# Performance work log

Measured on AMD Instinct MI355X. Metric: run time of the kernel, lower is better.

The kernel has to match this reference:

```python
import jax, jax.numpy as jnp
import numpy as np

H = 64          # heightmap size (sqrt of in_channels=4096)
FEATS = [8, 16, 32, 64]
NEG_SLOPE = 0.01
EPS = 1e-12


def setup_inputs() -> dict:
    key = jax.random.key(0)
    ks = jax.random.split(key, 32)
    inp = {"x": jax.random.normal(ks[0], (16384, H * H), dtype=jnp.float32)}
    in_feat = H
    ki = 1
    for li, out_feat in enumerate(FEATS):
        bound = np.sqrt(6.0 / (in_feat + out_feat))  # xavier_uniform
        inp[f"w{li}"] = jax.random.uniform(ks[ki], (out_feat, in_feat), minval=-bound, maxval=bound, dtype=jnp.float32); ki += 1
        inp[f"b{li}"] = jnp.zeros((out_feat,), dtype=jnp.float32)
        inp[f"s{li}"] = jnp.ones((1,), dtype=jnp.float32)  # sigma parameter
        in_feat = out_feat
    compress_in = H * FEATS[-1]
    inp["wm0"] = jax.random.normal(ks[ki], (80, compress_in), dtype=jnp.float32) * 0.02; ki += 1
    inp["bm0"] = jnp.zeros((80,), dtype=jnp.float32)
    inp["wm1"] = jax.random.normal(ks[ki], (60, 80), dtype=jnp.float32) * 0.02; ki += 1
    inp["bm1"] = jnp.zeros((60,), dtype=jnp.float32)
    return inp


def _gauss_layer(x, dist_sq, sigma, w, b):
    # x: [B, H, Cin] ; dist_sq: [H, H] ; w: [Cout, Cin]
    xp = jnp.einsum('bhc,oc->bho', x, w) + b
    k = jnp.exp(-dist_sq / (2.0 * sigma[0] ** 2))                 # [H, H]
    k = k / jnp.maximum(jnp.sum(k, axis=-1, keepdims=True), EPS)  # L1 normalize
    out = jnp.einsum('ij,bjc->bic', k, xp)
    return jax.nn.leaky_relu(out, NEG_SLOPE)


def reference(x, w0, b0, s0, w1, b1, s1, w2, b2, s2, w3, b3, s3, wm0, bm0, wm1, bm1):
    B = x.shape[0]
    h = x.reshape(B, H, H)
    idx = jnp.arange(H, dtype=x.dtype)
    dist_sq = (idx[:, None] - idx[None, :]) ** 2  # coords are 1-D row indices
    for sigma, w, b in ((s0, w0, b0), (s1, w1, b1), (s2, w2, b2), (s3, w3, b3)):
        h = _gauss_layer(h, dist_sq, sigma, w, b)
    h = h.reshape(B, -1)                              # [B, H*64]
    h = jax.nn.leaky_relu(h @ wm0.T + bm0, NEG_SLOPE)
    h = jax.nn.leaky_relu(h @ wm1.T + bm1, NEG_SLOPE)
    return h
```

## Files before the change

kernel.cpp:

```cpp
#include <hip/hip_runtime.h>


typedef _Float16 f16x8 __attribute__((ext_vector_type(8)));
typedef _Float16 f16x4 __attribute__((ext_vector_type(4)));
typedef float    f32x4 __attribute__((ext_vector_type(4)));

#define KT_OFF    327680
#define W0P_OFF   344064
#define W1P_OFF   345088
#define W2P_OFF   345600
#define W3P_OFF   346624

__global__ void prep_all(const float* __restrict__ s0, const float* __restrict__ s1,
                         const float* __restrict__ s2, const float* __restrict__ s3,
                         const float* __restrict__ w0, const float* __restrict__ w1,
                         const float* __restrict__ w2, const float* __restrict__ w3,
                         const float* __restrict__ wm0, _Float16* __restrict__ base) {
  int bid = blockIdx.x, tid = threadIdx.x;
  if (bid < 1280) {
    int idx = bid * 256 + tid;
    int kc = idx / 2560, rem = idx % 2560;
    int n = rem >> 5, o = rem & 31;
    base[idx] = (_Float16)wm0[n * 4096 + kc * 32 + o];
  } else if (bid == 1280) {
    int li = tid >> 6, i = tid & 63;
    float sg = (li == 0) ? s0[0] : (li == 1) ? s1[0] : (li == 2) ? s2[0] : s3[0];
    float denom = 2.0f * sg * sg;
    float sum = 0.0f;
    for (int j = 0; j < 64; ++j) {
      float d = (float)(i - j);
      sum += expf(-(d * d) / denom);
    }
    float inv = 1.0f / fmaxf(sum, 1e-12f);
    for (int j = 0; j < 64; ++j) {
      float d = (float)(i - j);
      base[KT_OFF + (li * 64 + i) * 64 + j] = (_Float16)(expf(-(d * d) / denom) * inv);
    }
  } else {
    for (int r = tid; r < 4608; r += 256) {
      float v;
      if (r < 1024)      { int o = r >> 6, c = r & 63;             v = (o < 8)  ? w0[o * 64 + c] : 0.0f; }
      else if (r < 1536) { int q = r - 1024; int o = q >> 5, c = q & 31; v = (c < 8)  ? w1[o * 8 + c]  : 0.0f; }
      else if (r < 2560) { int q = r - 1536; int o = q >> 5, c = q & 31; v = (c < 16) ? w2[o * 16 + c] : 0.0f; }
      else               { int q = r - 2560; int o = q >> 5, c = q & 31; v = w3[o * 32 + c]; }
      base[W0P_OFF + r] = (_Float16)v;
    }
  }
}

__device__ __forceinline__ float leaky(float v) { return v > 0.0f ? v : 0.01f * v; }

__device__ __forceinline__ int swz(int sx, int row, int c) {
  return row * 64 + ((((c >> 3) ^ (row & 7) ^ sx) & 7) << 3) + (c & 7);
}

template<int NT, int KC, int KPAD>
__device__ __forceinline__ void stage_a(_Float16* __restrict__ P, int sx,
                                        const _Float16* __restrict__ wp, const float* bv,
                                        int lo, int hi) {
  f16x8 a[4][KC];
#pragma unroll
  for (int mt = 0; mt < 4; ++mt)
#pragma unroll
    for (int kc = 0; kc < KC; ++kc)
      a[mt][kc] = *(const f16x8*)(P + swz(sx, mt * 16 + lo, kc * 32 + hi * 8));
  f16x8 wf[NT][KC];
#pragma unroll
  for (int nt = 0; nt < NT; ++nt)
#pragma unroll
    for (int kc = 0; kc < KC; ++kc)
      wf[nt][kc] = *(const f16x8*)(wp + (nt * 16 + lo) * KPAD + kc * 32 + hi * 8);
#pragma unroll
  for (int mt = 0; mt < 4; ++mt)
#pragma unroll
    for (int nt = 0; nt < NT; ++nt) {
      f32x4 acc = {0.0f, 0.0f, 0.0f, 0.0f};
#pragma unroll
      for (int kc = 0; kc < KC; ++kc)
        acc = __builtin_amdgcn_mfma_f32_16x16x32_f16(a[mt][kc], wf[nt][kc], acc, 0, 0, 0);
      f16x4 hv;
#pragma unroll
      for (int r = 0; r < 4; ++r) hv[r] = (_Float16)(acc[r] + bv[nt]);
      *(f16x4*)(P + swz(sx, nt * 16 + lo, mt * 16 + hi * 4)) = hv;
    }
}

template<int MT>
__device__ __forceinline__ void stage_b(_Float16* __restrict__ P, int sx,
                                        const _Float16* __restrict__ kmat, int lo, int hi) {
  f16x8 ax[MT][2];
#pragma unroll
  for (int ot = 0; ot < MT; ++ot)
#pragma unroll
    for (int kc = 0; kc < 2; ++kc)
      ax[ot][kc] = *(const f16x8*)(P + swz(sx, ot * 16 + lo, kc * 32 + hi * 8));
  f16x8 kb[4][2];
#pragma unroll
  for (int nt = 0; nt < 4; ++nt)
#pragma unroll
    for (int kc = 0; kc < 2; ++kc)
      kb[nt][kc] = *(const f16x8*)(kmat + (nt * 16 + lo) * 64 + kc * 32 + hi * 8);
#pragma unroll
  for (int ot = 0; ot < MT; ++ot)
#pragma unroll
    for (int nt = 0; nt < 4; ++nt) {
      f32x4 acc = {0.0f, 0.0f, 0.0f, 0.0f};
#pragma unroll
      for (int kc = 0; kc < 2; ++kc)
        acc = __builtin_amdgcn_mfma_f32_16x16x32_f16(ax[ot][kc], kb[nt][kc], acc, 0, 0, 0);
      f16x4 hv;
#pragma unroll
      for (int r = 0; r < 4; ++r) hv[r] = (_Float16)leaky(acc[r]);
      *(f16x4*)(P + swz(sx, nt * 16 + lo, ot * 16 + hi * 4)) = hv;
    }
}

__global__ __launch_bounds__(512, 4)
void fused(const float* __restrict__ x,
           const float* __restrict__ bb0, const float* __restrict__ bb1,
           const float* __restrict__ bb2, const float* __restrict__ bb3,
           const _Float16* __restrict__ wsh,
           const float* __restrict__ bm0, const float* __restrict__ wm1,
           const float* __restrict__ bm1, float* __restrict__ out, int B) {
  __shared__ _Float16 lds[8][4096];
  const int tid = threadIdx.x;
  const int wv = tid >> 6, lane = tid & 63;
  const int lo = lane & 15, hi = lane >> 4;
  const int smp0 = blockIdx.x * 8;
  int smp = smp0 + wv;
  if (smp >= B) smp = B - 1;
  _Float16* P = lds[wv];
  const int sx = wv;

  float bv0 = (lo < 8) ? bb0[lo] : 0.0f;
  float bv1 = bb1[lo];
  float bv2[2] = {bb2[lo], bb2[16 + lo]};
  float bv3[4] = {bb3[lo], bb3[16 + lo], bb3[32 + lo], bb3[48 + lo]};

  const float4* xv = (const float4*)(x + (size_t)smp * 4096);
#pragma unroll
  for (int t = 0; t < 16; ++t) {
    float4 v = xv[t * 64 + lane];
    f16x4 hv;
    hv[0] = (_Float16)v.x; hv[1] = (_Float16)v.y; hv[2] = (_Float16)v.z; hv[3] = (_Float16)v.w;
    *(f16x4*)(P + swz(sx, t * 4 + hi, lo * 4)) = hv;
  }

  const _Float16* kt = wsh + KT_OFF;
  stage_a<1, 2, 64>(P, sx, wsh + W0P_OFF, &bv0, lo, hi);
  stage_b<1>(P, sx, kt + 0 * 4096, lo, hi);
  stage_a<1, 1, 32>(P, sx, wsh + W1P_OFF, &bv1, lo, hi);
  stage_b<1>(P, sx, kt + 1 * 4096, lo, hi);
  stage_a<2, 1, 32>(P, sx, wsh + W2P_OFF, bv2, lo, hi);
  stage_b<2>(P, sx, kt + 2 * 4096, lo, hi);
  stage_a<4, 1, 32>(P, sx, wsh + W3P_OFF, bv3, lo, hi);
  stage_b<4>(P, sx, kt + 3 * 4096, lo, hi);

  __syncthreads();

  f32x4 acc[5];
#pragma unroll
  for (int nt = 0; nt < 5; ++nt) { f32x4 z = {0.0f, 0.0f, 0.0f, 0.0f}; acc[nt] = z; }

  const _Float16* ap = &lds[lo & 7][0];
#pragma unroll 2
  for (int it = 0; it < 16; ++it) {
    int kc = wv * 16 + it;
    int row = kc >> 1, cc = (kc & 1) * 32 + hi * 8;
    f16x8 a = *(const f16x8*)(ap + swz(lo & 7, row, cc));
    const _Float16* bp = wsh + (size_t)kc * 2560 + lo * 32 + hi * 8;
#pragma unroll
    for (int nt = 0; nt < 5; ++nt) {
      f16x8 b = *(const f16x8*)(bp + nt * 512);
      acc[nt] = __builtin_amdgcn_mfma_f32_16x16x32_f16(a, b, acc[nt], 0, 0, 0);
    }
  }
  __syncthreads();

  float* scr = (float*)&lds[0][0];
  if (hi < 2) {
#pragma unroll
    for (int nt = 0; nt < 5; ++nt)
#pragma unroll
      for (int r = 0; r < 4; ++r)
        scr[wv * 640 + (hi * 4 + r) * 80 + nt * 16 + lo] = acc[nt][r];
  }
  __syncthreads();

  float* h1 = scr + 5120;
  for (int e = tid; e < 640; e += 512) {
    int m = e / 80, n = e - m * 80;
    float v = bm0[n];
#pragma unroll
    for (int w = 0; w < 8; ++w) v += scr[w * 640 + e];
    h1[e] = leaky(v);
  }
  __syncthreads();

  if (tid < 480) {
    int m = tid / 60, n = tid - m * 60;
    float v = bm1[n];
    const float4* hr = (const float4*)(h1 + m * 80);
    const float4* wr = (const float4*)(wm1 + n * 80);
#pragma unroll
    for (int k2 = 0; k2 < 20; ++k2) {
      float4 hv = hr[k2], wv4 = wr[k2];
      v += hv.x * wv4.x + hv.y * wv4.y + hv.z * wv4.z + hv.w * wv4.w;
    }
    int s = smp0 + m;
    if (s < B) out[(size_t)s * 60 + n] = leaky(v);
  }
}

extern "C" void kernel_launch(void* const* d_in, const int* in_sizes, int n_in,
                              void* d_out, int out_size, void* d_ws, size_t ws_size,
                              hipStream_t stream) {
  const float* x   = (const float*)d_in[0];
  const float* w0  = (const float*)d_in[1];
  const float* b0  = (const float*)d_in[2];
  const float* s0  = (const float*)d_in[3];
  const float* w1  = (const float*)d_in[4];
  const float* b1  = (const float*)d_in[5];
  const float* s1  = (const float*)d_in[6];
  const float* w2  = (const float*)d_in[7];
  const float* b2  = (const float*)d_in[8];
  const float* s2  = (const float*)d_in[9];
  const float* w3  = (const float*)d_in[10];
  const float* b3  = (const float*)d_in[11];
  const float* s3  = (const float*)d_in[12];
  const float* wm0 = (const float*)d_in[13];
  const float* bm0 = (const float*)d_in[14];
  const float* wm1 = (const float*)d_in[15];
  const float* bm1 = (const float*)d_in[16];
  float* out = (float*)d_out;
  _Float16* wsh = (_Float16*)d_ws;

  int B = in_sizes[0] / 4096;

  prep_all<<<1282, 256, 0, stream>>>(s0, s1, s2, s3, w0, w1, w2, w3, wm0, wsh);
  fused<<<(B + 7) / 8, 512, 0, stream>>>(x, b0, b1, b2, b3, wsh, bm0, wm1, bm1, out, B);
}
```

Baseline: 189.0 us.

## Split each sample's Gauss-layer chain across two waves with block barriers

Blocks grow to 1024 threads so two wavefronts share each sample. Each wave does half the x load, half the output tiles of every projection and smoothing stage, and half the compress-GEMM k-chunks. Block-wide barriers around every stage keep the shared LDS buffer consistent. The aim is more parallelism per sample and shorter per-wave register and latency chains, at the cost of many extra __syncthreads per block and reduced blocks per CU.

```diff
diff --git a/kernel.cpp b/kernel.cpp
--- a/kernel.cpp
+++ b/kernel.cpp
@@ -55,67 +55,71 @@
 }
 
 template<int NT, int KC, int KPAD>
-__device__ __forceinline__ void stage_a(_Float16* __restrict__ P, int sx,
-                                        const _Float16* __restrict__ wp, const float* bv,
-                                        int lo, int hi) {
-  f16x8 a[4][KC];
-#pragma unroll
-  for (int mt = 0; mt < 4; ++mt)
+__device__ __forceinline__ void stage_a2(_Float16* __restrict__ P, int sx, int half,
+                                         const _Float16* __restrict__ wp, const float* bv,
+                                         int lo, int hi) {
+  f16x8 a[2][KC];
+#pragma unroll
+  for (int m = 0; m < 2; ++m)
 #pragma unroll
     for (int kc = 0; kc < KC; ++kc)
-      a[mt][kc] = *(const f16x8*)(P + swz(sx, mt * 16 + lo, kc * 32 + hi * 8));
+      a[m][kc] = *(const f16x8*)(P + swz(sx, (half * 2 + m) * 16 + lo, kc * 32 + hi * 8));
   f16x8 wf[NT][KC];
 #pragma unroll
   for (int nt = 0; nt < NT; ++nt)
 #pragma unroll
     for (int kc = 0; kc < KC; ++kc)
       wf[nt][kc] = *(const f16x8*)(wp + (nt * 16 + lo) * KPAD + kc * 32 + hi * 8);
-#pragma unroll
-  for (int mt = 0; mt < 4; ++mt)
+  __syncthreads();
+#pragma unroll
+  for (int m = 0; m < 2; ++m)
 #pragma unroll
     for (int nt = 0; nt < NT; ++nt) {
       f32x4 acc = {0.0f, 0.0f, 0.0f, 0.0f};
 #pragma unroll
       for (int kc = 0; kc < KC; ++kc)
-        acc = __builtin_amdgcn_mfma_f32_16x16x32_f16(a[mt][kc], wf[nt][kc], acc, 0, 0, 0);
+        acc = __builtin_amdgcn_mfma_f32_16x16x32_f16(a[m][kc], wf[nt][kc], acc, 0, 0, 0);
       f16x4 hv;
 #pragma unroll
       for (int r = 0; r < 4; ++r) hv[r] = (_Float16)(acc[r] + bv[nt]);
-      *(f16x4*)(P + swz(sx, nt * 16 + lo, mt * 16 + hi * 4)) = hv;
-    }
+      *(f16x4*)(P + swz(sx, nt * 16 + lo, (half * 2 + m) * 16 + hi * 4)) = hv;
+    }
+  __syncthreads();
 }
 
 template<int MT>
-__device__ __forceinline__ void stage_b(_Float16* __restrict__ P, int sx,
-                                        const _Float16* __restrict__ kmat, int lo, int hi) {
+__device__ __forceinline__ void stage_b2(_Float16* __restrict__ P, int sx, int half,
+                                         const _Float16* __restrict__ kmat, int lo, int hi) {
   f16x8 ax[MT][2];
 #pragma unroll
   for (int ot = 0; ot < MT; ++ot)
 #pragma unroll
     for (int kc = 0; kc < 2; ++kc)
       ax[ot][kc] = *(const f16x8*)(P + swz(sx, ot * 16 + lo, kc * 32 + hi * 8));
-  f16x8 kb[4][2];
-#pragma unroll
-  for (int nt = 0; nt < 4; ++nt)
+  f16x8 kb[2][2];
+#pragma unroll
+  for (int n = 0; n < 2; ++n)
 #pragma unroll
     for (int kc = 0; kc < 2; ++kc)
-      kb[nt][kc] = *(const f16x8*)(kmat + (nt * 16 + lo) * 64 + kc * 32 + hi * 8);
+      kb[n][kc] = *(const f16x8*)(kmat + ((half * 2 + n) * 16 + lo) * 64 + kc * 32 + hi * 8);
+  __syncthreads();
 #pragma unroll
   for (int ot = 0; ot < MT; ++ot)
 #pragma unroll
-    for (int nt = 0; nt < 4; ++nt) {
+    for (int n = 0; n < 2; ++n) {
       f32x4 acc = {0.0f, 0.0f, 0.0f, 0.0f};
 #pragma unroll
       for (int kc = 0; kc < 2; ++kc)
-        acc = __builtin_amdgcn_mfma_f32_16x16x32_f16(ax[ot][kc], kb[nt][kc], acc, 0, 0, 0);
+        acc = __builtin_amdgcn_mfma_f32_16x16x32_f16(ax[ot][kc], kb[n][kc], acc, 0, 0, 0);
       f16x4 hv;
 #pragma unroll
       for (int r = 0; r < 4; ++r) hv[r] = (_Float16)leaky(acc[r]);
-      *(f16x4*)(P + swz(sx, nt * 16 + lo, ot * 16 + hi * 4)) = hv;
-    }
-}
-
-__global__ __launch_bounds__(512, 4)
+      *(f16x4*)(P + swz(sx, (half * 2 + n) * 16 + lo, ot * 16 + hi * 4)) = hv;
+    }
+  __syncthreads();
+}
+
+__global__ __launch_bounds__(1024, 6)
 void fused(const float* __restrict__ x,
            const float* __restrict__ bb0, const float* __restrict__ bb1,
            const float* __restrict__ bb2, const float* __restrict__ bb3,
@@ -126,11 +130,12 @@
   const int tid = threadIdx.x;
   const int wv = tid >> 6, lane = tid & 63;
   const int lo = lane & 15, hi = lane >> 4;
+  const int sample = wv >> 1, half = wv & 1;
   const int smp0 = blockIdx.x * 8;
-  int smp = smp0 + wv;
+  int smp = smp0 + sample;
   if (smp >= B) smp = B - 1;
-  _Float16* P = lds[wv];
-  const int sx = wv;
+  _Float16* P = lds[sample];
+  const int sx = sample;
 
   float bv0 = (lo < 8) ? bb0[lo] : 0.0f;
   float bv1 = bb1[lo];
@@ -139,24 +144,24 @@
 
   const float4* xv = (const float4*)(x + (size_t)smp * 4096);
 #pragma unroll
-  for (int t = 0; t < 16; ++t) {
+  for (int tt = 0; tt < 8; ++tt) {
+    int t = half * 8 + tt;
     float4 v = xv[t * 64 + lane];
     f16x4 hv;
     hv[0] = (_Float16)v.x; hv[1] = (_Float16)v.y; hv[2] = (_Float16)v.z; hv[3] = (_Float16)v.w;
     *(f16x4*)(P + swz(sx, t * 4 + hi, lo * 4)) = hv;
   }
+  __syncthreads();
 
   const _Float16* kt = wsh + KT_OFF;
-  stage_a<1, 2, 64>(P, sx, wsh + W0P_OFF, &bv0, lo, hi);
-  stage_b<1>(P, sx, kt + 0 * 4096, lo, hi);
-  stage_a<1, 1, 32>(P, sx, wsh + W1P_OFF, &bv1, lo, hi);
-  stage_b<1>(P, sx, kt + 1 * 4096, lo, hi);
-  stage_a<2, 1, 32>(P, sx, wsh + W2P_OFF, bv2, lo, hi);
-  stage_b<2>(P, sx, kt + 2 * 4096, lo, hi);
-  stage_a<4, 1, 32>(P, sx, wsh + W3P_OFF, bv3, lo, hi);
-  stage_b<4>(P, sx, kt + 3 * 4096, lo, hi);
-
-  __syncthreads();
+  stage_a2<1, 2, 64>(P, sx, half, wsh + W0P_OFF, &bv0, lo, hi);
+  stage_b2<1>(P, sx, half, kt + 0 * 4096, lo, hi);
+  stage_a2<1, 1, 32>(P, sx, half, wsh + W1P_OFF, &bv1, lo, hi);
+  stage_b2<1>(P, sx, half, kt + 1 * 4096, lo, hi);
+  stage_a2<2, 1, 32>(P, sx, half, wsh + W2P_OFF, bv2, lo, hi);
+  stage_b2<2>(P, sx, half, kt + 2 * 4096, lo, hi);
+  stage_a2<4, 1, 32>(P, sx, half, wsh + W3P_OFF, bv3, lo, hi);
+  stage_b2<4>(P, sx, half, kt + 3 * 4096, lo, hi);
 
   f32x4 acc[5];
 #pragma unroll
@@ -164,8 +169,8 @@
 
   const _Float16* ap = &lds[lo & 7][0];
 #pragma unroll 2
-  for (int it = 0; it < 16; ++it) {
-    int kc = wv * 16 + it;
+  for (int it = 0; it < 8; ++it) {
+    int kc = wv * 8 + it;
     int row = kc >> 1, cc = (kc & 1) * 32 + hi * 8;
     f16x8 a = *(const f16x8*)(ap + swz(lo & 7, row, cc));
     const _Float16* bp = wsh + (size_t)kc * 2560 + lo * 32 + hi * 8;
@@ -187,12 +192,12 @@
   }
   __syncthreads();
 
-  float* h1 = scr + 5120;
-  for (int e = tid; e < 640; e += 512) {
+  float* h1 = scr + 10240;
+  for (int e = tid; e < 640; e += 1024) {
     int m = e / 80, n = e - m * 80;
     float v = bm0[n];
 #pragma unroll
-    for (int w = 0; w < 8; ++w) v += scr[w * 640 + e];
+    for (int w = 0; w < 16; ++w) v += scr[w * 640 + e];
     h1[e] = leaky(v);
   }
   __syncthreads();
@@ -238,5 +243,5 @@
   int B = in_sizes[0] / 4096;
 
   prep_all<<<1282, 256, 0, stream>>>(s0, s1, s2, s3, w0, w1, w2, w3, wm0, wsh);
-  fused<<<(B + 7) / 8, 512, 0, stream>>>(x, b0, b1, b2, b3, wsh, bm0, wm1, bm1, out, B);
-}
+  fused<<<(B + 7) / 8, 1024, 0, stream>>>(x, b0, b1, b2, b3, wsh, bm0, wm1, bm1, out, B);
+}
```

New measurement: 268.6 us. 1.42x slower.

## Process two samples per wave to fill the MFMA M-tile and share weight loads

Applied to the files above, without the earlier changes.

Each wave now handles two samples at once, interleaving their MFMA chains through the gauss and projection stages. Weight and kernel fragments are loaded once and reused for both samples. In the compression GEMM, the 16 MFMA rows now map to 16 real samples instead of 8 duplicated ones. In exchange, LDS use per block doubles to 128KB and the launch bound drops to 2 blocks per CU, which lowers occupancy and raises register pressure. Scheduling barriers are added around the load phases.

```diff
diff --git a/kernel.cpp b/kernel.cpp
--- a/kernel.cpp
+++ b/kernel.cpp
@@ -55,106 +55,135 @@
 }
 
 template<int NT, int KC, int KPAD>
-__device__ __forceinline__ void stage_a(_Float16* __restrict__ P, int sx,
-                                        const _Float16* __restrict__ wp, const float* bv,
-                                        int lo, int hi) {
-  f16x8 a[4][KC];
+__device__ __forceinline__ void stage_a_dual(_Float16* PA, _Float16* PB,
+                                             int sxA, int sxB,
+                                             const _Float16* wp, const float* bv,
+                                             int lo, int hi) {
+  __builtin_amdgcn_sched_barrier(0);
+  f16x8 aA[4][KC], aB[4][KC];
 #pragma unroll
   for (int mt = 0; mt < 4; ++mt)
 #pragma unroll
-    for (int kc = 0; kc < KC; ++kc)
-      a[mt][kc] = *(const f16x8*)(P + swz(sx, mt * 16 + lo, kc * 32 + hi * 8));
+    for (int kc = 0; kc < KC; ++kc) {
+      aA[mt][kc] = *(const f16x8*)(PA + swz(sxA, mt * 16 + lo, kc * 32 + hi * 8));
+      aB[mt][kc] = *(const f16x8*)(PB + swz(sxB, mt * 16 + lo, kc * 32 + hi * 8));
+    }
   f16x8 wf[NT][KC];
 #pragma unroll
   for (int nt = 0; nt < NT; ++nt)
 #pragma unroll
     for (int kc = 0; kc < KC; ++kc)
       wf[nt][kc] = *(const f16x8*)(wp + (nt * 16 + lo) * KPAD + kc * 32 + hi * 8);
+  __builtin_amdgcn_sched_barrier(0);
 #pragma unroll
   for (int mt = 0; mt < 4; ++mt)
 #pragma unroll
     for (int nt = 0; nt < NT; ++nt) {
-      f32x4 acc = {0.0f, 0.0f, 0.0f, 0.0f};
-#pragma unroll
-      for (int kc = 0; kc < KC; ++kc)
-        acc = __builtin_amdgcn_mfma_f32_16x16x32_f16(a[mt][kc], wf[nt][kc], acc, 0, 0, 0);
-      f16x4 hv;
-#pragma unroll
-      for (int r = 0; r < 4; ++r) hv[r] = (_Float16)(acc[r] + bv[nt]);
-      *(f16x4*)(P + swz(sx, nt * 16 + lo, mt * 16 + hi * 4)) = hv;
+      f32x4 accA = {0.0f, 0.0f, 0.0f, 0.0f};
+      f32x4 accB = {0.0f, 0.0f, 0.0f, 0.0f};
+#pragma unroll
+      for (int kc = 0; kc < KC; ++kc) {
+        accA = __builtin_amdgcn_mfma_f32_16x16x32_f16(aA[mt][kc], wf[nt][kc], accA, 0, 0, 0);
+        accB = __builtin_amdgcn_mfma_f32_16x16x32_f16(aB[mt][kc], wf[nt][kc], accB, 0, 0, 0);
+      }
+      f16x4 hA, hB;
+#pragma unroll
+      for (int r = 0; r < 4; ++r) {
+        hA[r] = (_Float16)(accA[r] + bv[nt]);
+        hB[r] = (_Float16)(accB[r] + bv[nt]);
+      }
+      *(f16x4*)(PA + swz(sxA, nt * 16 + lo, mt * 16 + hi * 4)) = hA;
+      *(f16x4*)(PB + swz(sxB, nt * 16 + lo, mt * 16 + hi * 4)) = hB;
     }
 }
 
 template<int MT>
-__device__ __forceinline__ void stage_b(_Float16* __restrict__ P, int sx,
-                                        const _Float16* __restrict__ kmat, int lo, int hi) {
-  f16x8 ax[MT][2];
+__device__ __forceinline__ void stage_b_dual(_Float16* PA, _Float16* PB,
+                                             int sxA, int sxB,
+                                             const _Float16* kmat, int lo, int hi) {
+  __builtin_amdgcn_sched_barrier(0);
+  f16x8 axA[MT][2], axB[MT][2];
 #pragma unroll
   for (int ot = 0; ot < MT; ++ot)
 #pragma unroll
-    for (int kc = 0; kc < 2; ++kc)
-      ax[ot][kc] = *(const f16x8*)(P + swz(sx, ot * 16 + lo, kc * 32 + hi * 8));
+    for (int kc = 0; kc < 2; ++kc) {
+      axA[ot][kc] = *(const f16x8*)(PA + swz(sxA, ot * 16 + lo, kc * 32 + hi * 8));
+      axB[ot][kc] = *(const f16x8*)(PB + swz(sxB, ot * 16 + lo, kc * 32 + hi * 8));
+    }
   f16x8 kb[4][2];
 #pragma unroll
   for (int nt = 0; nt < 4; ++nt)
 #pragma unroll
     for (int kc = 0; kc < 2; ++kc)
       kb[nt][kc] = *(const f16x8*)(kmat + (nt * 16 + lo) * 64 + kc * 32 + hi * 8);
+  __builtin_amdgcn_sched_barrier(0);
 #pragma unroll
   for (int ot = 0; ot < MT; ++ot)
 #pragma unroll
     for (int nt = 0; nt < 4; ++nt) {
-      f32x4 acc = {0.0f, 0.0f, 0.0f, 0.0f};
-#pragma unroll
-      for (int kc = 0; kc < 2; ++kc)
-        acc = __builtin_amdgcn_mfma_f32_16x16x32_f16(ax[ot][kc], kb[nt][kc], acc, 0, 0, 0);
-      f16x4 hv;
-#pragma unroll
-      for (int r = 0; r < 4; ++r) hv[r] = (_Float16)leaky(acc[r]);
-      *(f16x4*)(P + swz(sx, nt * 16 + lo, ot * 16 + hi * 4)) = hv;
-    }
-}
-
-__global__ __launch_bounds__(512, 4)
+      f32x4 accA = {0.0f, 0.0f, 0.0f, 0.0f};
+      f32x4 accB = {0.0f, 0.0f, 0.0f, 0.0f};
+#pragma unroll
+      for (int kc = 0; kc < 2; ++kc) {
+        accA = __builtin_amdgcn_mfma_f32_16x16x32_f16(axA[ot][kc], kb[nt][kc], accA, 0, 0, 0);
+        accB = __builtin_amdgcn_mfma_f32_16x16x32_f16(axB[ot][kc], kb[nt][kc], accB, 0, 0, 0);
+      }
+      f16x4 hA, hB;
+#pragma unroll
+      for (int r = 0; r < 4; ++r) {
+        hA[r] = (_Float16)leaky(accA[r]);
+        hB[r] = (_Float16)leaky(accB[r]);
+      }
+      *(f16x4*)(PA + swz(sxA, nt * 16 + lo, ot * 16 + hi * 4)) = hA;
+      *(f16x4*)(PB + swz(sxB, nt * 16 + lo, ot * 16 + hi * 4)) = hB;
+    }
+}
+
+__global__ __launch_bounds__(512, 2)
 void fused(const float* __restrict__ x,
            const float* __restrict__ bb0, const float* __restrict__ bb1,
            const float* __restrict__ bb2, const float* __restrict__ bb3,
            const _Float16* __restrict__ wsh,
            const float* __restrict__ bm0, const float* __restrict__ wm1,
            const float* __restrict__ bm1, float* __restrict__ out, int B) {
-  __shared__ _Float16 lds[8][4096];
+  __shared__ _Float16 lds[16][4096];
   const int tid = threadIdx.x;
   const int wv = tid >> 6, lane = tid & 63;
   const int lo = lane & 15, hi = lane >> 4;
-  const int smp0 = blockIdx.x * 8;
-  int smp = smp0 + wv;
-  if (smp >= B) smp = B - 1;
-  _Float16* P = lds[wv];
-  const int sx = wv;
+  const int smp0 = blockIdx.x * 16;
+  int smpA = smp0 + wv;      if (smpA >= B) smpA = B - 1;
+  int smpB = smp0 + wv + 8;  if (smpB >= B) smpB = B - 1;
+  _Float16* PA = lds[wv];
+  _Float16* PB = lds[wv + 8];
+  const int sxA = wv, sxB = wv + 8;
 
   float bv0 = (lo < 8) ? bb0[lo] : 0.0f;
   float bv1 = bb1[lo];
   float bv2[2] = {bb2[lo], bb2[16 + lo]};
   float bv3[4] = {bb3[lo], bb3[16 + lo], bb3[32 + lo], bb3[48 + lo]};
 
-  const float4* xv = (const float4*)(x + (size_t)smp * 4096);
+  const float4* xvA = (const float4*)(x + (size_t)smpA * 4096);
+  const float4* xvB = (const float4*)(x + (size_t)smpB * 4096);
 #pragma unroll
   for (int t = 0; t < 16; ++t) {
-    float4 v = xv[t * 64 + lane];
-    f16x4 hv;
-    hv[0] = (_Float16)v.x; hv[1] = (_Float16)v.y; hv[2] = (_Float16)v.z; hv[3] = (_Float16)v.w;
-    *(f16x4*)(P + swz(sx, t * 4 + hi, lo * 4)) = hv;
+    float4 vA = xvA[t * 64 + lane];
+    float4 vB = xvB[t * 64 + lane];
+    f16x4 hA, hB;
+    hA[0] = (_Float16)vA.x; hA[1] = (_Float16)vA.y; hA[2] = (_Float16)vA.z; hA[3] = (_Float16)vA.w;
+    hB[0] = (_Float16)vB.x; hB[1] = (_Float16)vB.y; hB[2] = (_Float16)vB.z; hB[3] = (_Float16)vB.w;
+    *(f16x4*)(PA + swz(sxA, t * 4 + hi, lo * 4)) = hA;
+    *(f16x4*)(PB + swz(sxB, t * 4 + hi, lo * 4)) = hB;
   }
 
   const _Float16* kt = wsh + KT_OFF;
-  stage_a<1, 2, 64>(P, sx, wsh + W0P_OFF, &bv0, lo, hi);
-  stage_b<1>(P, sx, kt + 0 * 4096, lo, hi);
-  stage_a<1, 1, 32>(P, sx, wsh + W1P_OFF, &bv1, lo, hi);
-  stage_b<1>(P, sx, kt + 1 * 4096, lo, hi);
-  stage_a<2, 1, 32>(P, sx, wsh + W2P_OFF, bv2, lo, hi);
-  stage_b<2>(P, sx, kt + 2 * 4096, lo, hi);
-  stage_a<4, 1, 32>(P, sx, wsh + W3P_OFF, bv3, lo, hi);
-  stage_b<4>(P, sx, kt + 3 * 4096, lo, hi);
+  stage_a_dual<1, 2, 64>(PA, PB, sxA, sxB, wsh + W0P_OFF, &bv0, lo, hi);
+  stage_b_dual<1>(PA, PB, sxA, sxB, kt + 0 * 4096, lo, hi);
+  stage_a_dual<1, 1, 32>(PA, PB, sxA, sxB, wsh + W1P_OFF, &bv1, lo, hi);
+  stage_b_dual<1>(PA, PB, sxA, sxB, kt + 1 * 4096, lo, hi);
+  stage_a_dual<2, 1, 32>(PA, PB, sxA, sxB, wsh + W2P_OFF, bv2, lo, hi);
+  stage_b_dual<2>(PA, PB, sxA, sxB, kt + 2 * 4096, lo, hi);
+  stage_a_dual<4, 1, 32>(PA, PB, sxA, sxB, wsh + W3P_OFF, bv3, lo, hi);
+  stage_b_dual<4>(PA, PB, sxA, sxB, kt + 3 * 4096, lo, hi);
 
   __syncthreads();
 
@@ -162,12 +191,12 @@
 #pragma unroll
   for (int nt = 0; nt < 5; ++nt) { f32x4 z = {0.0f, 0.0f, 0.0f, 0.0f}; acc[nt] = z; }
 
-  const _Float16* ap = &lds[lo & 7][0];
+  const _Float16* ap = &lds[lo][0];
 #pragma unroll 2
   for (int it = 0; it < 16; ++it) {
     int kc = wv * 16 + it;
     int row = kc >> 1, cc = (kc & 1) * 32 + hi * 8;
-    f16x8 a = *(const f16x8*)(ap + swz(lo & 7, row, cc));
+    f16x8 a = *(const f16x8*)(ap + swz(lo, row, cc));
     const _Float16* bp = wsh + (size_t)kc * 2560 + lo * 32 + hi * 8;
 #pragma unroll
     for (int nt = 0; nt < 5; ++nt) {
@@ -178,27 +207,25 @@
   __syncthreads();
 
   float* scr = (float*)&lds[0][0];
-  if (hi < 2) {
-#pragma unroll
-    for (int nt = 0; nt < 5; ++nt)
-#pragma unroll
-      for (int r = 0; r < 4; ++r)
-        scr[wv * 640 + (hi * 4 + r) * 80 + nt * 16 + lo] = acc[nt][r];
-  }
-  __syncthreads();
-
-  float* h1 = scr + 5120;
-  for (int e = tid; e < 640; e += 512) {
+#pragma unroll
+  for (int nt = 0; nt < 5; ++nt)
+#pragma unroll
+    for (int r = 0; r < 4; ++r)
+      scr[wv * 1280 + (hi * 4 + r) * 80 + nt * 16 + lo] = acc[nt][r];
+  __syncthreads();
+
+  float* h1 = scr + 10240;
+  for (int e = tid; e < 1280; e += 512) {
     int m = e / 80, n = e - m * 80;
     float v = bm0[n];
 #pragma unroll
-    for (int w = 0; w < 8; ++w) v += scr[w * 640 + e];
+    for (int w = 0; w < 8; ++w) v += scr[w * 1280 + e];
     h1[e] = leaky(v);
   }
   __syncthreads();
 
-  if (tid < 480) {
-    int m = tid / 60, n = tid - m * 60;
+  for (int e = tid; e < 960; e += 512) {
+    int m = e / 60, n = e - m * 60;
     float v = bm1[n];
     const float4* hr = (const float4*)(h1 + m * 80);
     const float4* wr = (const float4*)(wm1 + n * 80);
@@ -238,5 +265,5 @@
   int B = in_sizes[0] / 4096;
 
   prep_all<<<1282, 256, 0, stream>>>(s0, s1, s2, s3, w0, w1, w2, w3, wm0, wsh);
-  fused<<<(B + 7) / 8, 512, 0, stream>>>(x, b0, b1, b2, b3, wsh, bm0, wm1, bm1, out, B);
-}
+  fused<<<(B + 15) / 16, 512, 0, stream>>>(x, b0, b1, b2, b3, wsh, bm0, wm1, bm1, out, B);
+}
```

Result: faster. 166.7 us (-11.8%).

## Fuse first layer into global load, double block to 16 samples, add sched barriers

Applied to the files above, without the earlier changes.

Layer 0's A operand now comes directly from global x in MFMA fragment layout with inline f16 conversion. This removes the LDS staging write and read of the raw input. Blocks grow to 1024 threads handling 16 samples, so each wave does 8 K-chunks of the compress GEMM instead of 16, and all lanes now write partials to scratch. sched_barrier fences pin the LDS load batches ahead of the MFMAs, and the LDS tile is zeroed first. This raises LDS use per block to 128KB, which may limit occupancy, and the fragment-pattern global loads may coalesce less well.

```diff
diff --git a/kernel.cpp b/kernel.cpp
--- a/kernel.cpp
+++ b/kernel.cpp
@@ -54,10 +54,13 @@
   return row * 64 + ((((c >> 3) ^ (row & 7) ^ sx) & 7) << 3) + (c & 7);
 }
 
+#define DS_FENCE() __builtin_amdgcn_sched_barrier(0x7F)
+
 template<int NT, int KC, int KPAD>
-__device__ __forceinline__ void stage_a(_Float16* __restrict__ P, int sx,
-                                        const _Float16* __restrict__ wp, const float* bv,
-                                        int lo, int hi) {
+__device__ __forceinline__ void stage_a1(_Float16* P, int sx,
+                                         const _Float16* wp, const float* bv,
+                                         int lo, int hi) {
+  DS_FENCE();
   f16x8 a[4][KC];
 #pragma unroll
   for (int mt = 0; mt < 4; ++mt)
@@ -70,6 +73,7 @@
 #pragma unroll
     for (int kc = 0; kc < KC; ++kc)
       wf[nt][kc] = *(const f16x8*)(wp + (nt * 16 + lo) * KPAD + kc * 32 + hi * 8);
+  DS_FENCE();
 #pragma unroll
   for (int mt = 0; mt < 4; ++mt)
 #pragma unroll
@@ -86,8 +90,9 @@
 }
 
 template<int MT>
-__device__ __forceinline__ void stage_b(_Float16* __restrict__ P, int sx,
-                                        const _Float16* __restrict__ kmat, int lo, int hi) {
+__device__ __forceinline__ void stage_b1(_Float16* P, int sx,
+                                         const _Float16* kmat, int lo, int hi) {
+  DS_FENCE();
   f16x8 ax[MT][2];
 #pragma unroll
   for (int ot = 0; ot < MT; ++ot)
@@ -100,6 +105,7 @@
 #pragma unroll
     for (int kc = 0; kc < 2; ++kc)
       kb[nt][kc] = *(const f16x8*)(kmat + (nt * 16 + lo) * 64 + kc * 32 + hi * 8);
+  DS_FENCE();
 #pragma unroll
   for (int ot = 0; ot < MT; ++ot)
 #pragma unroll
@@ -115,46 +121,72 @@
     }
 }
 
-__global__ __launch_bounds__(512, 4)
+__global__ __launch_bounds__(1024, 4)
 void fused(const float* __restrict__ x,
            const float* __restrict__ bb0, const float* __restrict__ bb1,
            const float* __restrict__ bb2, const float* __restrict__ bb3,
            const _Float16* __restrict__ wsh,
            const float* __restrict__ bm0, const float* __restrict__ wm1,
            const float* __restrict__ bm1, float* __restrict__ out, int B) {
-  __shared__ _Float16 lds[8][4096];
+  __shared__ _Float16 lds[16][4096];
   const int tid = threadIdx.x;
   const int wv = tid >> 6, lane = tid & 63;
   const int lo = lane & 15, hi = lane >> 4;
-  const int smp0 = blockIdx.x * 8;
-  int smp = smp0 + wv;
-  if (smp >= B) smp = B - 1;
+  const int smp0 = blockIdx.x * 16;
+  int smp = smp0 + wv;  if (smp >= B) smp = B - 1;
   _Float16* P = lds[wv];
   const int sx = wv;
+
+  {
+    f16x8 z = {};
+#pragma unroll
+    for (int t = 0; t < 8; ++t)
+      *(f16x8*)(P + t * 512 + lane * 8) = z;
+  }
 
   float bv0 = (lo < 8) ? bb0[lo] : 0.0f;
   float bv1 = bb1[lo];
   float bv2[2] = {bb2[lo], bb2[16 + lo]};
   float bv3[4] = {bb3[lo], bb3[16 + lo], bb3[32 + lo], bb3[48 + lo]};
 
-  const float4* xv = (const float4*)(x + (size_t)smp * 4096);
-#pragma unroll
-  for (int t = 0; t < 16; ++t) {
-    float4 v = xv[t * 64 + lane];
+  const float* xr = x + (size_t)smp * 4096;
+  f16x8 a0[4][2];
+#pragma unroll
+  for (int mt = 0; mt < 4; ++mt)
+#pragma unroll
+    for (int kc = 0; kc < 2; ++kc) {
+      const float4* p4 = (const float4*)(xr + (mt * 16 + lo) * 64 + kc * 32 + hi * 8);
+      float4 v0 = p4[0], v1 = p4[1];
+      f16x8 a;
+      a[0] = (_Float16)v0.x; a[1] = (_Float16)v0.y; a[2] = (_Float16)v0.z; a[3] = (_Float16)v0.w;
+      a[4] = (_Float16)v1.x; a[5] = (_Float16)v1.y; a[6] = (_Float16)v1.z; a[7] = (_Float16)v1.w;
+      a0[mt][kc] = a;
+    }
+  f16x8 wf0[2];
+#pragma unroll
+  for (int kc = 0; kc < 2; ++kc)
+    wf0[kc] = *(const f16x8*)(wsh + W0P_OFF + lo * 64 + kc * 32 + hi * 8);
+  DS_FENCE();
+#pragma unroll
+  for (int mt = 0; mt < 4; ++mt) {
+    f32x4 acc = {0.0f, 0.0f, 0.0f, 0.0f};
+#pragma unroll
+    for (int kc = 0; kc < 2; ++kc)
+      acc = __builtin_amdgcn_mfma_f32_16x16x32_f16(a0[mt][kc], wf0[kc], acc, 0, 0, 0);
     f16x4 hv;
-    hv[0] = (_Float16)v.x; hv[1] = (_Float16)v.y; hv[2] = (_Float16)v.z; hv[3] = (_Float16)v.w;
-    *(f16x4*)(P + swz(sx, t * 4 + hi, lo * 4)) = hv;
+#pragma unroll
+    for (int r = 0; r < 4; ++r) hv[r] = (_Float16)(acc[r] + bv0);
+    *(f16x4*)(P + swz(sx, lo, mt * 16 + hi * 4)) = hv;
   }
 
   const _Float16* kt = wsh + KT_OFF;
-  stage_a<1, 2, 64>(P, sx, wsh + W0P_OFF, &bv0, lo, hi);
-  stage_b<1>(P, sx, kt + 0 * 4096, lo, hi);
-  stage_a<1, 1, 32>(P, sx, wsh + W1P_OFF, &bv1, lo, hi);
-  stage_b<1>(P, sx, kt + 1 * 4096, lo, hi);
-  stage_a<2, 1, 32>(P, sx, wsh + W2P_OFF, bv2, lo, hi);
-  stage_b<2>(P, sx, kt + 2 * 4096, lo, hi);
-  stage_a<4, 1, 32>(P, sx, wsh + W3P_OFF, bv3, lo, hi);
-  stage_b<4>(P, sx, kt + 3 * 4096, lo, hi);
+  stage_b1<1>(P, sx, kt + 0 * 4096, lo, hi);
+  stage_a1<1, 1, 32>(P, sx, wsh + W1P_OFF, &bv1, lo, hi);
+  stage_b1<1>(P, sx, kt + 1 * 4096, lo, hi);
+  stage_a1<2, 1, 32>(P, sx, wsh + W2P_OFF, bv2, lo, hi);
+  stage_b1<2>(P, sx, kt + 2 * 4096, lo, hi);
+  stage_a1<4, 1, 32>(P, sx, wsh + W3P_OFF, bv3, lo, hi);
+  stage_b1<4>(P, sx, kt + 3 * 4096, lo, hi);
 
   __syncthreads();
 
@@ -162,12 +194,12 @@
 #pragma unroll
   for (int nt = 0; nt < 5; ++nt) { f32x4 z = {0.0f, 0.0f, 0.0f, 0.0f}; acc[nt] = z; }
 
-  const _Float16* ap = &lds[lo & 7][0];
+  const _Float16* ap = &lds[lo][0];
 #pragma unroll 2
-  for (int it = 0; it < 16; ++it) {
-    int kc = wv * 16 + it;
+  for (int it = 0; it < 8; ++it) {
+    int kc = wv * 8 + it;
     int row = kc >> 1, cc = (kc & 1) * 32 + hi * 8;
-    f16x8 a = *(const f16x8*)(ap + swz(lo & 7, row, cc));
+    f16x8 a = *(const f16x8*)(ap + swz(lo, row, cc));
     const _Float16* bp = wsh + (size_t)kc * 2560 + lo * 32 + hi * 8;
 #pragma unroll
     for (int nt = 0; nt < 5; ++nt) {
@@ -178,27 +210,25 @@
   __syncthreads();
 
   float* scr = (float*)&lds[0][0];
-  if (hi < 2) {
-#pragma unroll
-    for (int nt = 0; nt < 5; ++nt)
-#pragma unroll
-      for (int r = 0; r < 4; ++r)
-        scr[wv * 640 + (hi * 4 + r) * 80 + nt * 16 + lo] = acc[nt][r];
-  }
-  __syncthreads();
-
-  float* h1 = scr + 5120;
-  for (int e = tid; e < 640; e += 512) {
+#pragma unroll
+  for (int nt = 0; nt < 5; ++nt)
+#pragma unroll
+    for (int r = 0; r < 4; ++r)
+      scr[wv * 1280 + (hi * 4 + r) * 80 + nt * 16 + lo] = acc[nt][r];
+  __syncthreads();
+
+  float* h1 = scr + 20480;
+  for (int e = tid; e < 1280; e += 1024) {
     int m = e / 80, n = e - m * 80;
     float v = bm0[n];
 #pragma unroll
-    for (int w = 0; w < 8; ++w) v += scr[w * 640 + e];
+    for (int w = 0; w < 16; ++w) v += scr[w * 1280 + e];
     h1[e] = leaky(v);
   }
   __syncthreads();
 
-  if (tid < 480) {
-    int m = tid / 60, n = tid - m * 60;
+  for (int e = tid; e < 960; e += 1024) {
+    int m = e / 60, n = e - m * 60;
     float v = bm1[n];
     const float4* hr = (const float4*)(h1 + m * 80);
     const float4* wr = (const float4*)(wm1 + n * 80);
@@ -238,5 +268,5 @@
   int B = in_sizes[0] / 4096;
 
   prep_all<<<1282, 256, 0, stream>>>(s0, s1, s2, s3, w0, w1, w2, w3, wm0, wsh);
-  fused<<<(B + 7) / 8, 512, 0, stream>>>(x, b0, b1, b2, b3, wsh, bm0, wm1, bm1, out, B);
-}
+  fused<<<(B + 15) / 16, 1024, 0, stream>>>(x, b0, b1, b2, b3, wsh, bm0, wm1, bm1, out, B);
+}
```

New measurement: 179.4 us. -5.1%, faster.
